# Performance work log

Measured on AMD Instinct MI355X. Metric: run time of the kernel, lower is better.

Reference implementation:

```python
import jax, jax.numpy as jnp
import numpy as np

B = 8192
CNN_DIM = 2048
MLP_DIM = 2048
HID = 1024
H = 16
D = HID // H  # 64
EPS = 1e-5


def setup_inputs() -> dict:
    key = jax.random.key(0)
    ks = jax.random.split(key, 12)
    s = 0.02
    return {
        'cnn_out': jax.random.normal(ks[0], (B, CNN_DIM), jnp.float32),
        'mlp_out': jax.random.normal(ks[1], (B, MLP_DIM), jnp.float32),
        # weights stored [in, out] (transposed vs torch nn.Linear)
        'W_cqkv': jax.random.normal(ks[2], (CNN_DIM, 3 * HID), jnp.float32) * s,
        'b_cqkv': jnp.zeros((3 * HID,), jnp.float32),
        'W_mqkv': jax.random.normal(ks[3], (MLP_DIM, 3 * HID), jnp.float32) * s,
        'b_mqkv': jnp.zeros((3 * HID,), jnp.float32),
        'g1': jnp.ones((HID,), jnp.float32),
        'be1': jnp.zeros((HID,), jnp.float32),
        'g2': jnp.ones((HID,), jnp.float32),
        'be2': jnp.zeros((HID,), jnp.float32),
        'W_cproj': jax.random.normal(ks[4], (HID, CNN_DIM), jnp.float32) * s,
        'b_cproj': jnp.zeros((CNN_DIM,), jnp.float32),
        'W_mproj': jax.random.normal(ks[5], (HID, MLP_DIM), jnp.float32) * s,
        'b_mproj': jnp.zeros((MLP_DIM,), jnp.float32),
    }


def _layernorm(x, g, b):
    m = jnp.mean(x, axis=-1, keepdims=True)
    v = jnp.mean((x - m) ** 2, axis=-1, keepdims=True)
    return (x - m) / jnp.sqrt(v + EPS) * g + b


def reference(cnn_out, mlp_out, W_cqkv, b_cqkv, W_mqkv, b_mqkv,
              g1, be1, g2, be2, W_cproj, b_cproj, W_mproj, b_mproj):
    bsz = cnn_out.shape[0]
    scale = 1.0 / jnp.sqrt(jnp.float32(D))

    cqkv = (cnn_out @ W_cqkv + b_cqkv).reshape(bsz, 3, H, D)
    cq, ck, cv = cqkv[:, 0], cqkv[:, 1], cqkv[:, 2]  # each [B,H,D]
    mqkv = (mlp_out @ W_mqkv + b_mqkv).reshape(bsz, 3, H, D)
    mq, mk, mv = mqkv[:, 0], mqkv[:, 1], mqkv[:, 2]

    # branch 1: cnn queries attend over mlp heads -> [B,H,H]
    a1 = jax.nn.softmax(jnp.einsum('bhd,bgd->bhg', cq, mk) * scale, axis=-1)
    ca = jnp.einsum('bhg,bgd->bhd', a1, mv)
    # torch: transpose(1,2).view(B, hidden) -> [B, D, H] flattened
    ca = jnp.swapaxes(ca, 1, 2).reshape(bsz, HID)
    cnn_enh = cnn_out + _layernorm(ca, g1, be1) @ W_cproj + b_cproj

    # branch 2: mlp queries attend over cnn heads
    a2 = jax.nn.softmax(jnp.einsum('bhd,bgd->bhg', mq, ck) * scale, axis=-1)
    ma = jnp.einsum('bhg,bgd->bhd', a2, cv)
    ma = jnp.swapaxes(ma, 1, 2).reshape(bsz, HID)
    mlp_enh = mlp_out + _layernorm(ma, g2, be2) @ W_mproj + b_mproj

    return (cnn_enh, mlp_enh)
```

## Files before the change

kernel.cpp:

```cpp
#include <hip/hip_runtime.h>
#include <hip/hip_bf16.h>
#include <cstdint>
#include <cstddef>

#define NROWS 8192
#define DIM   2048
#define HIDN  1024
#define QKV3  3072
#define EPSV  1e-5f

typedef __attribute__((ext_vector_type(8))) short bf16x8;
typedef __attribute__((ext_vector_type(8))) unsigned short u16x8;
typedef __attribute__((ext_vector_type(4))) float f32x4;

__device__ __forceinline__ unsigned short f2bf(float x) {
    __hip_bfloat16 h = __float2bfloat16(x);
    return *reinterpret_cast<unsigned short*>(&h);
}
__device__ __forceinline__ float bf2f(unsigned short u) {
    return __uint_as_float((unsigned)u << 16);
}

__device__ __forceinline__ void gload_lds16(const void* g, void* l) {
    __builtin_amdgcn_global_load_lds(
        (const __attribute__((address_space(1))) void*)g,
        (__attribute__((address_space(3))) void*)l, 16, 0, 0);
}

template <int N> __device__ __forceinline__ void vmwait() {
    if constexpr (N == 8)      asm volatile("s_waitcnt vmcnt(8)" ::: "memory");
    else if constexpr (N == 4) asm volatile("s_waitcnt vmcnt(4)" ::: "memory");
    else if constexpr (N == 2) asm volatile("s_waitcnt vmcnt(2)" ::: "memory");
    else if constexpr (N == 0) asm volatile("s_waitcnt vmcnt(0)" ::: "memory");
}
__device__ __forceinline__ void barrier_mem() {
    asm volatile("s_barrier" ::: "memory");
}

__global__ __launch_bounds__(256) void prep(
    const float* __restrict__ cnn, unsigned short* __restrict__ Abf_c,
    const float* __restrict__ mlp, unsigned short* __restrict__ Abf_m,
    const float* __restrict__ Wcq, unsigned short* __restrict__ WqT_c,
    const float* __restrict__ Wmq, unsigned short* __restrict__ WqT_m,
    const float* __restrict__ Wcp, unsigned short* __restrict__ WpT_c,
    const float* __restrict__ Wmp, unsigned short* __restrict__ WpT_m) {
    __shared__ float tile[32][129];
    const int bid = blockIdx.x;
    const int t = threadIdx.x;
    if (bid < 16384) {
        const int which = bid >> 13;
        const long b = bid & 8191;
        const float* in = which ? mlp : cnn;
        unsigned short* out = which ? Abf_m : Abf_c;
        const long base = (b * 256 + t) * 8;
        float4 a = *(const float4*)(in + base);
        float4 v = *(const float4*)(in + base + 4);
        uint4 r;
        r.x = (unsigned)f2bf(a.x) | ((unsigned)f2bf(a.y) << 16);
        r.y = (unsigned)f2bf(a.z) | ((unsigned)f2bf(a.w) << 16);
        r.z = (unsigned)f2bf(v.x) | ((unsigned)f2bf(v.y) << 16);
        r.w = (unsigned)f2bf(v.z) | ((unsigned)f2bf(v.w) << 16);
        *(uint4*)(out + base) = r;
        return;
    }
    int l = bid - 16384;
    const float* in;
    unsigned short* out;
    int R, C, nbc;
    if (l < 3072) {
        const int wq = l >> 11;
        const int wqq = l / 1536;
        l -= wqq * 1536;
        in = wqq ? Wmq : Wcq; out = wqq ? WqT_m : WqT_c; R = DIM; C = QKV3; nbc = 96;
        (void)wq;
    } else {
        l -= 3072;
        const int wp = l / 512;
        l -= wp * 512;
        in = wp ? Wmp : Wcp; out = wp ? WpT_m : WpT_c; R = HIDN; C = DIM; nbc = 64;
    }
    const int c0 = (l % nbc) * 32, r0 = (l / nbc) * 128;
#pragma unroll
    for (int i = 0; i < 16; ++i) {
        const int idx = t + i * 256;
        const int rr = idx >> 5, cc = idx & 31;
        tile[cc][rr] = in[(size_t)(r0 + rr) * C + c0 + cc];
    }
    __syncthreads();
#pragma unroll
    for (int k2 = 0; k2 < 2; ++k2) {
        const int u = t + k2 * 256;
        const int row = u >> 4, ch = u & 15;
        const float* p = &tile[row][ch * 8];
        u16x8 r;
#pragma unroll
        for (int k = 0; k < 8; ++k) r[k] = f2bf(p[k]);
        *(u16x8*)(out + (size_t)(c0 + row) * R + r0 + ch * 8) = r;
    }
}


__device__ __forceinline__ void stage_half(const unsigned short* __restrict__ G,
                                           int ldK, int rowBase, int kt,
                                           short* ldsHalf, int tid) {
#pragma unroll
    for (int i = 0; i < 2; ++i) {
        const int c = i * 512 + tid;
        const int r = c >> 3;
        const int jl = (c & 7) ^ (r & 7);
        const unsigned short* src = G + (size_t)(rowBase + r) * ldK + kt + jl * 8;
        char* dst = (char*)ldsHalf + (size_t)((i * 512 + (tid & 0x1C0)) * 16);
        gload_lds16(src, dst);
    }
}

__device__ __forceinline__ void load_a4(const short* sAb, int rowA, int o0, int mbase,
                                        bf16x8 (&a)[4][2]) {
#pragma unroll
    for (int m = 0; m < 4; ++m) {
        const char* p = (const char*)sAb + rowA + (mbase + m) * 4096;
        a[m][0] = *(const bf16x8*)(p + o0);
        a[m][1] = *(const bf16x8*)(p + (o0 ^ 64));
    }
}
__device__ __forceinline__ void load_b2(const short* sBb, int rowB, int o0, int nbase,
                                        bf16x8 (&b)[4][2]) {
#pragma unroll
    for (int n = 0; n < 2; ++n) {
        const char* p = (const char*)sBb + rowB + (nbase + n) * 8192;
        b[nbase + n][0] = *(const bf16x8*)(p + o0);
        b[nbase + n][1] = *(const bf16x8*)(p + (o0 ^ 64));
    }
}

#define QUAD(mq, nq)                                                          \
    __builtin_amdgcn_s_setprio(1);                                            \
    _Pragma("unroll") for (int kk_ = 0; kk_ < 2; ++kk_)                       \
    _Pragma("unroll") for (int n_ = 0; n_ < 2; ++n_)                          \
    _Pragma("unroll") for (int m_ = 0; m_ < 4; ++m_)                          \
        acc[(mq) + m_][(nq) + n_] = __builtin_amdgcn_mfma_f32_16x16x32_bf16(  \
            a[m_][kk_], b[(nq) + n_][kk_], acc[(mq) + m_][(nq) + n_], 0, 0, 0); \
    __builtin_amdgcn_s_setprio(0);

#define KTILE(BUF, MODE, KT1, KT2)                                            \
                                                                     \
    load_a4(&sA[BUF][0], rowA, o0, 0, a);                                     \
    if constexpr ((MODE) <= 1)                                                \
        stage_half(Bt, K, tn + 128, (KT1), &sB[(BUF) ^ 1][8192], tid);        \
    if constexpr ((MODE) == 2) { vmwait<2>(); } else { vmwait<8>(); }         \
    barrier_mem();                                                            \
    QUAD(0, 0);                                                               \
                                                                     \
    load_b2(&sB[BUF][0], rowB, o0, 2, b);                                     \
    if constexpr ((MODE) <= 1)                                                \
        stage_half(A, K, tm + 128, (KT1), &sA[(BUF) ^ 1][8192], tid);         \
    if constexpr ((MODE) == 2) { vmwait<0>(); } else { vmwait<8>(); }         \
    barrier_mem();                                                            \
    QUAD(0, 2);                                                               \
                                                                     \
    load_a4(&sA[BUF][0], rowA, o0, 4, a);                                     \
    if constexpr ((MODE) == 0)                                                \
        stage_half(A, K, tm, (KT2), &sA[BUF][0], tid);                        \
    barrier_mem();                                                            \
    QUAD(4, 0);                                                               \
                                                                     \
    if constexpr ((MODE) == 0) {                                              \
        stage_half(Bt, K, tn, (KT2), &sB[BUF][0], tid);                       \
        vmwait<8>();                                                          \
    }                                                                         \
    if constexpr ((MODE) == 1) { vmwait<4>(); }                               \
    barrier_mem();                                                            \
    if constexpr ((MODE) <= 1)                                                \
        load_b2(&sB[(BUF) ^ 1][0], rowB, o0, 0, b);   \
    QUAD(4, 2);

template <int EPI>
__global__ __launch_bounds__(512, 2) void gemm256(
    const unsigned short* __restrict__ A0, const unsigned short* __restrict__ B0t,
    const float* __restrict__ bias0, const float* __restrict__ res0, void* __restrict__ C0,
    const unsigned short* __restrict__ A1, const unsigned short* __restrict__ B1t,
    const float* __restrict__ bias1, const float* __restrict__ res1, void* __restrict__ C1,
    int M, int N, int K, int nbx) {
    __shared__ __align__(16) char smem[131072];
    short (*sA)[16384] = reinterpret_cast<short (*)[16384]>(smem);
    short (*sB)[16384] = reinterpret_cast<short (*)[16384]>(smem + 65536);
    float* smemF = reinterpret_cast<float*>(smem);

    const int tid = threadIdx.x;
    const int nwg = gridDim.x;
    const int ob = blockIdx.x;
    const int swz = (ob & 7) * (nwg >> 3) + (ob >> 3);
    const int per = nbx * (M >> 8);
    const int which = swz >= per ? 1 : 0;
    const int rem = swz - which * per;
    const int by = rem / nbx, bx = rem % nbx;
    const int tm = by << 8, tn = bx << 8;

    const unsigned short* __restrict__ A  = which ? A1 : A0;
    const unsigned short* __restrict__ Bt = which ? B1t : B0t;
    const float* __restrict__ bias  = which ? bias1 : bias0;
    const float* __restrict__ resid = which ? res1 : res0;

    const int w = tid >> 6, l = tid & 63;
    const int wm = w >> 2, wn = w & 3;
    const int lg = l >> 4, lr = l & 15;
    const int o0 = (lg ^ (lr & 7)) << 4;
    const int rowA = (16 * wm + lr) << 7;
    const int rowB = (16 * wn + lr) << 7;

    f32x4 acc[8][4] = {};
    bf16x8 a[4][2], b[4][2];

    const int T = K >> 6;

    stage_half(A,  K, tm,       0,  &sA[0][0],    tid);
    stage_half(Bt, K, tn,       0,  &sB[0][0],    tid);
    stage_half(Bt, K, tn + 128, 0,  &sB[0][8192], tid);
    stage_half(A,  K, tm + 128, 0,  &sA[0][8192], tid);
    stage_half(A,  K, tm,       64, &sA[1][0],    tid);
    stage_half(Bt, K, tn,       64, &sB[1][0],    tid);
    vmwait<8>();
    barrier_mem();
    load_b2(&sB[0][0], rowB, o0, 0, b);

    int kt = 0;
    for (int tt = 0; tt + 4 <= T; tt += 2) {
        KTILE(0, 0, kt + 64, kt + 128);
        KTILE(1, 0, kt + 128, kt + 192);
        kt += 128;
    }
    KTILE(0, 1, kt + 64, 0);
    KTILE(1, 2, 0, 0);

    barrier_mem();
    const int crow_l = 16 * wm + 4 * lg;
    const int ccol_l = 16 * wn + lr;
    const int cswz = lg << 3;
#pragma unroll
    for (int half = 0; half < 2; ++half) {
#pragma unroll
        for (int mi2 = 0; mi2 < 4; ++mi2) {
            const int lrow = 32 * mi2 + crow_l;
#pragma unroll
            for (int ni = 0; ni < 4; ++ni) {
                const int colg = ccol_l + 64 * ni;
                const float bb = bias[tn + colg];
                const f32x4 v = acc[half * 4 + mi2][ni];
                const int colp = colg ^ cswz;
#pragma unroll
                for (int j = 0; j < 4; ++j)
                    smemF[(lrow + j) * 256 + colp] = v[j] + bb;
            }
        }
        barrier_mem();
        const int rowb = tm + half * 128;
        if constexpr (EPI == 0) {
            unsigned short* C = (unsigned short*)(which ? C1 : C0);
#pragma unroll
            for (int i = 0; i < 8; ++i) {
                const int f8 = tid + i * 512;
                const int row = f8 >> 5, c8 = (f8 & 31) * 8;
                const int msk = ((row >> 2) & 3) << 3;
                const float* p = smemF + row * 256 + (c8 ^ msk);
                u16x8 r;
#pragma unroll
                for (int k = 0; k < 8; ++k) r[k] = f2bf(p[k]);
                *(u16x8*)(C + (size_t)(rowb + row) * N + tn + c8) = r;
            }
        } else {
            float* C = (float*)(which ? C1 : C0);
#pragma unroll
            for (int i = 0; i < 16; ++i) {
                const int f4 = tid + i * 512;
                const int row = f4 >> 6, c4 = (f4 & 63) * 4;
                const int msk = ((row >> 2) & 3) << 3;
                const size_t idx = (size_t)(rowb + row) * N + tn + c4;
                float4 v = *(const float4*)(smemF + row * 256 + (c4 ^ msk));
                const float4 rr = *(const float4*)(resid + idx);
                v.x += rr.x; v.y += rr.y; v.z += rr.z; v.w += rr.w;
                *(float4*)(C + idx) = v;
            }
        }
        barrier_mem();
    }
}

__device__ __forceinline__ void attn_path(const float* __restrict__ q,
                                          const float* __restrict__ k,
                                          const float* __restrict__ v,
                                          const float* __restrict__ gw,
                                          const float* __restrict__ bw,
                                          unsigned short* __restrict__ out, long b,
                                          float* sS, float* sP, float* red, int t) {
    const int h = t >> 4, gg = t & 15;
    const float* qr = q + h * 68;
    const float* kr = k + gg * 68;
    float s = 0.f;
#pragma unroll
    for (int d = 0; d < 64; d += 4) {
        const float4 qv = *(const float4*)(qr + d);
        const float4 kv = *(const float4*)(kr + d);
        s += qv.x * kv.x + qv.y * kv.y + qv.z * kv.z + qv.w * kv.w;
    }
    sS[h * 17 + gg] = s * 0.125f;
    __syncthreads();
    float mx = -1e30f;
#pragma unroll
    for (int j = 0; j < 16; ++j) mx = fmaxf(mx, sS[h * 17 + j]);
    float sum = 0.f;
#pragma unroll
    for (int j = 0; j < 16; ++j) sum += __expf(sS[h * 17 + j] - mx);
    const float aa = __expf(sS[h * 17 + gg] - mx) / sum;
    sP[h * 17 + gg] = aa;
    __syncthreads();
    float xs[4];
    float lsum = 0.f, lss = 0.f;
#pragma unroll
    for (int r = 0; r < 4; ++r) {
        const int i = t + 256 * r;
        const int d = i >> 4, hh = i & 15;
        float accv = 0.f;
#pragma unroll
        for (int g2 = 0; g2 < 16; ++g2) accv += sP[hh * 17 + g2] * v[g2 * 68 + d];
        xs[r] = accv;
        lsum += accv;
        lss += accv * accv;
    }
#pragma unroll
    for (int off = 32; off > 0; off >>= 1) {
        lsum += __shfl_down(lsum, off);
        lss += __shfl_down(lss, off);
    }
    if ((t & 63) == 0) {
        red[(t >> 6) * 2] = lsum;
        red[(t >> 6) * 2 + 1] = lss;
    }
    __syncthreads();
    const float tot = red[0] + red[2] + red[4] + red[6];
    const float tot2 = red[1] + red[3] + red[5] + red[7];
    const float mean = tot * (1.f / 1024.f);
    const float var = tot2 * (1.f / 1024.f) - mean * mean;
    const float rstd = rsqrtf(var + EPSV);
#pragma unroll
    for (int r = 0; r < 4; ++r) {
        const int i = t + 256 * r;
        const float y = (xs[r] - mean) * rstd * gw[i] + bw[i];
        out[b * 1024 + i] = f2bf(y);
    }
}

__global__ __launch_bounds__(256) void attn_ln(const unsigned short* __restrict__ qkv_c,
                                               const unsigned short* __restrict__ qkv_m,
                                               const float* __restrict__ g1,
                                               const float* __restrict__ be1,
                                               const float* __restrict__ g2,
                                               const float* __restrict__ be2,
                                               unsigned short* __restrict__ ln1,
                                               unsigned short* __restrict__ ln2) {
    __shared__ float qc[48 * 68];
    __shared__ float qm[48 * 68];
    __shared__ float sS[16 * 17];
    __shared__ float sP[16 * 17];
    __shared__ float red[8];
    const int t = threadIdx.x;
    const long b = blockIdx.x;

    const unsigned short* rc = qkv_c + b * QKV3;
    const unsigned short* rm = qkv_m + b * QKV3;
#pragma unroll
    for (int it = 0; it < 3; ++it) {
        const int i0 = t * 4 + it * 1024;
        ushort4 vc = *(const ushort4*)(rc + i0);
        ushort4 vm = *(const ushort4*)(rm + i0);
        const int o = (i0 >> 6) * 68 + (i0 & 63);
        qc[o + 0] = bf2f(vc.x); qc[o + 1] = bf2f(vc.y);
        qc[o + 2] = bf2f(vc.z); qc[o + 3] = bf2f(vc.w);
        qm[o + 0] = bf2f(vm.x); qm[o + 1] = bf2f(vm.y);
        qm[o + 2] = bf2f(vm.z); qm[o + 3] = bf2f(vm.w);
    }
    __syncthreads();
    attn_path(qc, qm + 16 * 68, qm + 32 * 68, g1, be1, ln1, b, sS, sP, red, t);
    __syncthreads();
    attn_path(qm, qc + 16 * 68, qc + 32 * 68, g2, be2, ln2, b, sS, sP, red, t);
}

extern "C" void kernel_launch(void* const* d_in, const int* in_sizes, int n_in,
                              void* d_out, int out_size, void* d_ws, size_t ws_size,
                              hipStream_t stream) {
    const float* cnn    = (const float*)d_in[0];
    const float* mlp    = (const float*)d_in[1];
    const float* W_cqkv = (const float*)d_in[2];
    const float* b_cqkv = (const float*)d_in[3];
    const float* W_mqkv = (const float*)d_in[4];
    const float* b_mqkv = (const float*)d_in[5];
    const float* g1     = (const float*)d_in[6];
    const float* be1    = (const float*)d_in[7];
    const float* g2     = (const float*)d_in[8];
    const float* be2    = (const float*)d_in[9];
    const float* W_cproj = (const float*)d_in[10];
    const float* b_cproj = (const float*)d_in[11];
    const float* W_mproj = (const float*)d_in[12];
    const float* b_mproj = (const float*)d_in[13];
    float* out = (float*)d_out;
    char* ws = (char*)d_ws;

    unsigned short* Abf_c = (unsigned short*)(ws + 0);
    unsigned short* Abf_m = (unsigned short*)(ws + 33554432);
    unsigned short* WqT_c = (unsigned short*)(ws + 67108864);
    unsigned short* WqT_m = (unsigned short*)(ws + 79691776);
    unsigned short* qkv_c = (unsigned short*)(ws + 92274688);
    unsigned short* qkv_m = (unsigned short*)(ws + 142606336);
    unsigned short* ln1   = (unsigned short*)(ws + 0);
    unsigned short* ln2   = (unsigned short*)(ws + 16777216);
    unsigned short* WpT_c = (unsigned short*)(ws + 192937984);
    unsigned short* WpT_m = (unsigned short*)(ws + 197132288);

    prep<<<20480, 256, 0, stream>>>(cnn, Abf_c, mlp, Abf_m,
                                    W_cqkv, WqT_c, W_mqkv, WqT_m,
                                    W_cproj, WpT_c, W_mproj, WpT_m);

    gemm256<0><<<768, 512, 0, stream>>>(Abf_c, WqT_c, b_cqkv, nullptr, qkv_c,
                                        Abf_m, WqT_m, b_mqkv, nullptr, qkv_m,
                                        NROWS, QKV3, DIM, QKV3 / 256);

    attn_ln<<<NROWS, 256, 0, stream>>>(qkv_c, qkv_m, g1, be1, g2, be2, ln1, ln2);

    gemm256<1><<<512, 512, 0, stream>>>(ln1, WpT_c, b_cproj, cnn, out,
                                        ln2, WpT_m, b_mproj, mlp, out + (size_t)NROWS * DIM,
                                        NROWS, DIM, HIDN, DIM / 256);
}
```

Before: 389.4 us.

## Run both attention branches concurrently in 512-thread blocks and drop LDS swizzle

```diff
diff --git a/kernel.cpp b/kernel.cpp
--- a/kernel.cpp
+++ b/kernel.cpp
@@ -68,11 +68,9 @@
     unsigned short* out;
     int R, C, nbc;
     if (l < 3072) {
-        const int wq = l >> 11;
         const int wqq = l / 1536;
         l -= wqq * 1536;
         in = wqq ? Wmq : Wcq; out = wqq ? WqT_m : WqT_c; R = DIM; C = QKV3; nbc = 96;
-        (void)wq;
     } else {
         l -= 3072;
         const int wp = l / 512;
@@ -235,7 +233,6 @@
     barrier_mem();
     const int crow_l = 16 * wm + 4 * lg;
     const int ccol_l = 16 * wn + lr;
-    const int cswz = lg << 3;
 #pragma unroll
     for (int half = 0; half < 2; ++half) {
 #pragma unroll
@@ -246,10 +243,9 @@
                 const int colg = ccol_l + 64 * ni;
                 const float bb = bias[tn + colg];
                 const f32x4 v = acc[half * 4 + mi2][ni];
-                const int colp = colg ^ cswz;
 #pragma unroll
                 for (int j = 0; j < 4; ++j)
-                    smemF[(lrow + j) * 256 + colp] = v[j] + bb;
+                    smemF[(lrow + j) * 256 + colg] = v[j] + bb;
             }
         }
         barrier_mem();
@@ -260,8 +256,7 @@
             for (int i = 0; i < 8; ++i) {
                 const int f8 = tid + i * 512;
                 const int row = f8 >> 5, c8 = (f8 & 31) * 8;
-                const int msk = ((row >> 2) & 3) << 3;
-                const float* p = smemF + row * 256 + (c8 ^ msk);
+                const float* p = smemF + row * 256 + c8;
                 u16x8 r;
 #pragma unroll
                 for (int k = 0; k < 8; ++k) r[k] = f2bf(p[k]);
@@ -273,9 +268,8 @@
             for (int i = 0; i < 16; ++i) {
                 const int f4 = tid + i * 512;
                 const int row = f4 >> 6, c4 = (f4 & 63) * 4;
-                const int msk = ((row >> 2) & 3) << 3;
                 const size_t idx = (size_t)(rowb + row) * N + tn + c4;
-                float4 v = *(const float4*)(smemF + row * 256 + (c4 ^ msk));
+                float4 v = *(const float4*)(smemF + row * 256 + c4);
                 const float4 rr = *(const float4*)(resid + idx);
                 v.x += rr.x; v.y += rr.y; v.z += rr.z; v.w += rr.w;
                 *(float4*)(C + idx) = v;
@@ -285,71 +279,7 @@
     }
 }
 
-__device__ __forceinline__ void attn_path(const float* __restrict__ q,
-                                          const float* __restrict__ k,
-                                          const float* __restrict__ v,
-                                          const float* __restrict__ gw,
-                                          const float* __restrict__ bw,
-                                          unsigned short* __restrict__ out, long b,
-                                          float* sS, float* sP, float* red, int t) {
-    const int h = t >> 4, gg = t & 15;
-    const float* qr = q + h * 68;
-    const float* kr = k + gg * 68;
-    float s = 0.f;
-#pragma unroll
-    for (int d = 0; d < 64; d += 4) {
-        const float4 qv = *(const float4*)(qr + d);
-        const float4 kv = *(const float4*)(kr + d);
-        s += qv.x * kv.x + qv.y * kv.y + qv.z * kv.z + qv.w * kv.w;
-    }
-    sS[h * 17 + gg] = s * 0.125f;
-    __syncthreads();
-    float mx = -1e30f;
-#pragma unroll
-    for (int j = 0; j < 16; ++j) mx = fmaxf(mx, sS[h * 17 + j]);
-    float sum = 0.f;
-#pragma unroll
-    for (int j = 0; j < 16; ++j) sum += __expf(sS[h * 17 + j] - mx);
-    const float aa = __expf(sS[h * 17 + gg] - mx) / sum;
-    sP[h * 17 + gg] = aa;
-    __syncthreads();
-    float xs[4];
-    float lsum = 0.f, lss = 0.f;
-#pragma unroll
-    for (int r = 0; r < 4; ++r) {
-        const int i = t + 256 * r;
-        const int d = i >> 4, hh = i & 15;
-        float accv = 0.f;
-#pragma unroll
-        for (int g2 = 0; g2 < 16; ++g2) accv += sP[hh * 17 + g2] * v[g2 * 68 + d];
-        xs[r] = accv;
-        lsum += accv;
-        lss += accv * accv;
-    }
-#pragma unroll
-    for (int off = 32; off > 0; off >>= 1) {
-        lsum += __shfl_down(lsum, off);
-        lss += __shfl_down(lss, off);
-    }
-    if ((t & 63) == 0) {
-        red[(t >> 6) * 2] = lsum;
-        red[(t >> 6) * 2 + 1] = lss;
-    }
-    __syncthreads();
-    const float tot = red[0] + red[2] + red[4] + red[6];
-    const float tot2 = red[1] + red[3] + red[5] + red[7];
-    const float mean = tot * (1.f / 1024.f);
-    const float var = tot2 * (1.f / 1024.f) - mean * mean;
-    const float rstd = rsqrtf(var + EPSV);
-#pragma unroll
-    for (int r = 0; r < 4; ++r) {
-        const int i = t + 256 * r;
-        const float y = (xs[r] - mean) * rstd * gw[i] + bw[i];
-        out[b * 1024 + i] = f2bf(y);
-    }
-}
-
-__global__ __launch_bounds__(256) void attn_ln(const unsigned short* __restrict__ qkv_c,
+__global__ __launch_bounds__(512) void attn_ln(const unsigned short* __restrict__ qkv_c,
                                                const unsigned short* __restrict__ qkv_m,
                                                const float* __restrict__ g1,
                                                const float* __restrict__ be1,
@@ -359,29 +289,96 @@
                                                unsigned short* __restrict__ ln2) {
     __shared__ float qc[48 * 68];
     __shared__ float qm[48 * 68];
-    __shared__ float sS[16 * 17];
-    __shared__ float sP[16 * 17];
-    __shared__ float red[8];
+    __shared__ float sS[2][16 * 17];
+    __shared__ float sP[2][16 * 17];
+    __shared__ float red[2][8];
     const int t = threadIdx.x;
     const long b = blockIdx.x;
-
-    const unsigned short* rc = qkv_c + b * QKV3;
-    const unsigned short* rm = qkv_m + b * QKV3;
-#pragma unroll
-    for (int it = 0; it < 3; ++it) {
-        const int i0 = t * 4 + it * 1024;
-        ushort4 vc = *(const ushort4*)(rc + i0);
-        ushort4 vm = *(const ushort4*)(rm + i0);
-        const int o = (i0 >> 6) * 68 + (i0 & 63);
-        qc[o + 0] = bf2f(vc.x); qc[o + 1] = bf2f(vc.y);
-        qc[o + 2] = bf2f(vc.z); qc[o + 3] = bf2f(vc.w);
-        qm[o + 0] = bf2f(vm.x); qm[o + 1] = bf2f(vm.y);
-        qm[o + 2] = bf2f(vm.z); qm[o + 3] = bf2f(vm.w);
+    const int p = t >> 8, tl = t & 255;
+
+    {
+        const unsigned short* src = (p ? qkv_m : qkv_c) + b * QKV3;
+        float* dst = p ? qm : qc;
+#pragma unroll
+        for (int it = 0; it < 3; ++it) {
+            const int i0 = tl * 4 + it * 1024;
+            ushort4 v4 = *(const ushort4*)(src + i0);
+            const int o = (i0 >> 6) * 68 + (i0 & 63);
+            dst[o + 0] = bf2f(v4.x); dst[o + 1] = bf2f(v4.y);
+            dst[o + 2] = bf2f(v4.z); dst[o + 3] = bf2f(v4.w);
+        }
     }
     __syncthreads();
-    attn_path(qc, qm + 16 * 68, qm + 32 * 68, g1, be1, ln1, b, sS, sP, red, t);
+
+    const float* q  = p ? qm : qc;
+    const float* kv = p ? qc : qm;
+    const float* k  = kv + 16 * 68;
+    const float* v  = kv + 32 * 68;
+    const float* gw = p ? g2 : g1;
+    const float* bw = p ? be2 : be1;
+    unsigned short* out = p ? ln2 : ln1;
+    float* mS = sS[p];
+    float* mP = sP[p];
+    float* mR = red[p];
+
+    const int h = tl >> 4, gg = tl & 15;
+    {
+        const float* qr = q + h * 68;
+        const float* kr = k + gg * 68;
+        float s = 0.f;
+#pragma unroll
+        for (int d = 0; d < 64; d += 4) {
+            const float4 qv = *(const float4*)(qr + d);
+            const float4 kvv = *(const float4*)(kr + d);
+            s += qv.x * kvv.x + qv.y * kvv.y + qv.z * kvv.z + qv.w * kvv.w;
+        }
+        mS[h * 17 + gg] = s * 0.125f;
+    }
     __syncthreads();
-    attn_path(qm, qc + 16 * 68, qc + 32 * 68, g2, be2, ln2, b, sS, sP, red, t);
+    {
+        float mx = -1e30f;
+#pragma unroll
+        for (int j = 0; j < 16; ++j) mx = fmaxf(mx, mS[h * 17 + j]);
+        float sum = 0.f;
+#pragma unroll
+        for (int j = 0; j < 16; ++j) sum += __expf(mS[h * 17 + j] - mx);
+        mP[h * 17 + gg] = __expf(mS[h * 17 + gg] - mx) / sum;
+    }
+    __syncthreads();
+    float xs[4];
+    float lsum = 0.f, lss = 0.f;
+#pragma unroll
+    for (int r = 0; r < 4; ++r) {
+        const int i = tl + 256 * r;
+        const int d = i >> 4, hh = i & 15;
+        float accv = 0.f;
+#pragma unroll
+        for (int g2i = 0; g2i < 16; ++g2i) accv += mP[hh * 17 + g2i] * v[g2i * 68 + d];
+        xs[r] = accv;
+        lsum += accv;
+        lss += accv * accv;
+    }
+#pragma unroll
+    for (int off = 32; off > 0; off >>= 1) {
+        lsum += __shfl_down(lsum, off);
+        lss += __shfl_down(lss, off);
+    }
+    if ((t & 63) == 0) {
+        mR[((t >> 6) & 3) * 2] = lsum;
+        mR[((t >> 6) & 3) * 2 + 1] = lss;
+    }
+    __syncthreads();
+    const float tot = mR[0] + mR[2] + mR[4] + mR[6];
+    const float tot2 = mR[1] + mR[3] + mR[5] + mR[7];
+    const float mean = tot * (1.f / 1024.f);
+    const float var = tot2 * (1.f / 1024.f) - mean * mean;
+    const float rstd = rsqrtf(var + EPSV);
+#pragma unroll
+    for (int r = 0; r < 4; ++r) {
+        const int i = tl + 256 * r;
+        const float y = (xs[r] - mean) * rstd * gw[i] + bw[i];
+        out[b * 1024 + i] = f2bf(y);
+    }
 }
 
 extern "C" void kernel_launch(void* const* d_in, const int* in_sizes, int n_in,
@@ -423,7 +420,7 @@
                                         Abf_m, WqT_m, b_mqkv, nullptr, qkv_m,
                                         NROWS, QKV3, DIM, QKV3 / 256);
 
-    attn_ln<<<NROWS, 256, 0, stream>>>(qkv_c, qkv_m, g1, be1, g2, be2, ln1, ln2);
+    attn_ln<<<NROWS, 512, 0, stream>>>(qkv_c, qkv_m, g1, be1, g2, be2, ln1, ln2);
 
     gemm256<1><<<512, 512, 0, stream>>>(ln1, WpT_c, b_cproj, cnn, out,
                                         ln2, WpT_m, b_mproj, mlp, out + (size_t)NROWS * DIM,
```

After: 389.5 us. About the same (+0.0%).
